# Optimization experiments

Hardware: AMD Instinct MI355X
Metric: run time of the kernel (lower is better)

## Reference

```python
import jax, jax.numpy as jnp
import numpy as np

HEAD_SIZE = 128


def setup_inputs() -> dict:
    key = jax.random.key(0)
    k0, k1, k2, k3 = jax.random.split(key, 4)
    B, S, E, H = 4, 4096, 1024, HEAD_SIZE
    x = jax.random.normal(k0, (B, S, E), dtype=jnp.float32)
    scale = 1.0 / np.sqrt(E).astype(np.float32)
    Wq = jax.random.normal(k1, (E, H), dtype=jnp.float32) * scale
    Wk = jax.random.normal(k2, (E, H), dtype=jnp.float32) * scale
    Wv = jax.random.normal(k3, (E, H), dtype=jnp.float32) * scale
    k_mask = jnp.ones((B, S), dtype=jnp.int32)
    return {"x": x, "Wq": Wq, "Wk": Wk, "Wv": Wv, "k_mask": k_mask}


def reference(x, Wq, Wk, Wv, k_mask):
    # Self-attention path (kv=None), causal=True
    Q = x @ Wq  # [B, S, H]
    K = x @ Wk  # [B, S, H]
    V = x @ Wv  # [B, S, H]
    inv_sqrt_h = np.float32(1.0 / np.sqrt(HEAD_SIZE))
    att = jnp.einsum('bqh,bkh->bqk', Q, K) * inv_sqrt_h  # [B, S, S]
    neg_inf = jnp.float32(-jnp.inf)
    # padding mask over keys: [B, 1, S_k]
    att = jnp.where(k_mask[:, None, :] == 0, neg_inf, att)
    # causal mask: tril over (q_len, k_len)
    S = Q.shape[1]
    c_mask = jnp.tril(jnp.ones((S, S), dtype=bool))  # [S, S]
    att = jnp.where(c_mask[None, :, :], att, neg_inf)
    att = jax.nn.softmax(att, axis=-1)
    return att @ V  # [B, S, H]
```

## Files before the change

### kernel.cpp

```cpp
#include <hip/hip_runtime.h>
#include <hip/hip_bf16.h>

typedef unsigned short u16;
typedef __attribute__((ext_vector_type(8))) short bf16x8;
typedef __attribute__((ext_vector_type(4))) float f32x4;
typedef __attribute__((ext_vector_type(4))) unsigned short u16x4;

#define SQ 4096
#define HQ 128
#define NCHUNK 144

__device__ __forceinline__ u16 f2b(float f) {
  unsigned int u = __float_as_uint(f);
  unsigned int r = (u + 0x7fffu + ((u >> 16) & 1u)) >> 16;
  return (u16)r;
}

__device__ __forceinline__ u16 f2b_fast(float f) {
  __hip_bfloat16 h = __float2bfloat16(f);
  return __builtin_bit_cast(u16, h);
}

__device__ __forceinline__ float b2f(u16 v) {
  unsigned int u = ((unsigned int)v) << 16;
  return __uint_as_float(u);
}

__device__ __forceinline__ void gload_lds16(const u16* gsrc, u16* ldst) {
  __builtin_amdgcn_global_load_lds((const __attribute__((address_space(1))) void*)gsrc,
                                   (__attribute__((address_space(3))) void*)ldst, 16, 0, 0);
}

__global__ __launch_bounds__(256) void k_wt(const float* __restrict__ Wq, const float* __restrict__ Wk,
                                            const float* __restrict__ Wv, u16* __restrict__ wt) {
  int idx = blockIdx.x * 256 + threadIdx.x;
  int z = idx >> 17, r = idx & 131071, n = r >> 10, k = r & 1023;
  const float* W = (z == 0) ? Wq : (z == 1) ? Wk : Wv;
  wt[idx] = f2b(W[k * 128 + n]);
}

__global__ __launch_bounds__(256, 3) void k_proj(const float* __restrict__ x, const u16* __restrict__ wt,
                                                 u16* __restrict__ qb, u16* __restrict__ kb,
                                                 u16* __restrict__ vt) {
  int blk = blockIdx.x;
  int t = threadIdx.x;
  int wn = t >> 6, lane = t & 63;
  int lr = lane & 15, lg = lane >> 4;

  __shared__ __align__(16) u16 xl[2][32 * 32];
  __shared__ __align__(16) u16 wl[2][384 * 32];

  int srow = t >> 3, sc8 = t & 7;
  const float* xg = x + (long)(blk * 32 + srow) * 1024 + sc8 * 4;
  int xch = ((sc8 >> 1) ^ ((srow >> 1) & 3));
  int xoff = srow * 32 + xch * 8 + (sc8 & 1) * 4;

  f32x4 acc[2][6];
#pragma unroll
  for (int i = 0; i < 2; ++i)
#pragma unroll
    for (int j = 0; j < 6; ++j) acc[i][j] = (f32x4){0.f, 0.f, 0.f, 0.f};

  auto stage_w = [&](int bufi, int k0) {
#pragma unroll
    for (int i = 0; i < 6; ++i) {
      int ci = i * 256 + t;
      int row = ci >> 2, ch = ci & 3;
      gload_lds16(wt + (long)row * 1024 + k0 + ((ch ^ ((row >> 1) & 3)) << 3),
                  &wl[bufi][0] + ci * 8);
    }
  };

  {
    float4 xa = *(const float4*)(xg);
    stage_w(0, 0);
    u16x4 o;
    o[0] = f2b(xa.x); o[1] = f2b(xa.y); o[2] = f2b(xa.z); o[3] = f2b(xa.w);
    *(u16x4*)(&xl[0][0] + xoff) = o;
  }
  __syncthreads();

  for (int ks = 0; ks < 32; ++ks) {
    int cur = ks & 1;
    float4 xa;
    bool more = (ks + 1 < 32);
    if (more) {
      xa = *(const float4*)(xg + (ks + 1) * 32);
      stage_w(cur ^ 1, (ks + 1) * 32);
    }
    bf16x8 af[2], bf[6];
#pragma unroll
    for (int i = 0; i < 2; ++i) {
      int row = i * 16 + lr;
      af[i] = *(const bf16x8*)(&xl[cur][0] + row * 32 + ((lg ^ ((row >> 1) & 3)) << 3));
    }
#pragma unroll
    for (int j = 0; j < 6; ++j) {
      int row = wn * 96 + j * 16 + lr;
      bf[j] = *(const bf16x8*)(&wl[cur][0] + row * 32 + ((lg ^ ((row >> 1) & 3)) << 3));
    }
#pragma unroll
    for (int i = 0; i < 2; ++i)
#pragma unroll
      for (int j = 0; j < 6; ++j)
        acc[i][j] = __builtin_amdgcn_mfma_f32_16x16x32_bf16(af[i], bf[j], acc[i][j], 0, 0, 0);
    if (more) {
      u16x4 o;
      o[0] = f2b(xa.x); o[1] = f2b(xa.y); o[2] = f2b(xa.z); o[3] = f2b(xa.w);
      *(u16x4*)(&xl[cur ^ 1][0] + xoff) = o;
    }
    __syncthreads();
  }

#pragma unroll
  for (int i = 0; i < 2; ++i)
#pragma unroll
    for (int j = 0; j < 6; ++j)
#pragma unroll
      for (int r = 0; r < 4; ++r) {
        int m = blk * 32 + i * 16 + lg * 4 + r;
        int col = wn * 96 + j * 16 + lr;
        int z = col >> 7, cz = col & 127;
        u16 v = f2b(acc[i][j][r]);
        if (z == 0) qb[(long)m * 128 + cz] = v;
        else if (z == 1) kb[(long)m * 128 + cz] = v;
        else { int bb = m >> 12, sR = m & 4095; vt[(long)bb * 524288 + (long)cz * 4096 + sR] = v; }
      }
}

__global__ __launch_bounds__(512, 4) void k_attn(const u16* __restrict__ qb, const u16* __restrict__ kb,
                                                 const u16* __restrict__ vt, const int* __restrict__ kmask,
                                                 u16* __restrict__ po, float* __restrict__ pl) {
  const float SCALE_LOG2 = 0.08838834764831845f * 1.4426950408889634f;
  const float MFIX = 24.0f;
  int f = (NCHUNK - 1) - (int)blockIdx.x;
  int b = blockIdx.y;
  int qt2 = 0, cum = 0;
  while (cum + ((qt2 + 4) >> 2) <= f) { cum += (qt2 + 4) >> 2; ++qt2; }
  int kc = f - cum;
  int ntile = 2 * qt2 + 2;
  int kt0 = kc * 8;
  int kt1 = min(kt0 + 8, ntile);

  int t = threadIdx.x, w = t >> 6, lane = t & 63;
  int lr = lane & 15, lg = lane >> 4, sw = lr & 7;
  int qrow0 = qt2 * 128 + w * 16;
  const u16* Q = qb + ((long)(b * SQ + qrow0)) * HQ;
  const u16* K = kb + (long)b * SQ * HQ;
  const u16* V = vt + (long)b * HQ * SQ;
  const int* msk = kmask + b * SQ;

  __shared__ __align__(16) u16 Kl[2][64 * 128];
  __shared__ __align__(16) u16 Vl[2][128 * 64];
  __shared__ __align__(16) u16 plds[8][16 * 64];

  bf16x8 aq[4];
#pragma unroll
  for (int c = 0; c < 4; ++c) aq[c] = *(const bf16x8*)(Q + lr * HQ + c * 32 + lg * 8);

  bf16x8 ones;
#pragma unroll
  for (int e = 0; e < 8; ++e) ones[e] = (short)0x3F80;

  f32x4 o[8];
#pragma unroll
  for (int n = 0; n < 8; ++n) o[n] = (f32x4){0.f, 0.f, 0.f, 0.f};
  f32x4 l_acc = (f32x4){0.f, 0.f, 0.f, 0.f};

  auto stage = [&](int bufi, int kb0) {
    const u16* Kg = K + (long)kb0 * HQ;
    const u16* Vg = V + kb0;
#pragma unroll
    for (int i = 0; i < 2; ++i) {
      int ci = w * 2 + i;
      int o16 = ci * 64 + lane;
      int row = o16 >> 4, ch = o16 & 15;
      gload_lds16(Kg + row * HQ + ((ch ^ (row & 7)) << 3), &Kl[bufi][ci * 512]);
    }
#pragma unroll
    for (int i = 0; i < 2; ++i) {
      int ci = w * 2 + i;
      int o16 = ci * 64 + lane;
      int row = o16 >> 3, ch = o16 & 7;
      gload_lds16(Vg + (long)row * SQ + ((ch ^ (row & 7)) << 3), &Vl[bufi][ci * 512]);
    }
  };

  stage(0, kt0 * 64);
  __syncthreads();

  u16* pw = &plds[w][0];
  for (int kt = kt0; kt < kt1; ++kt) {
    int cur = (kt - kt0) & 1;
    int kb0 = kt * 64;
    if (kt + 1 < kt1) stage(cur ^ 1, kb0 + 64);

    if (kb0 <= qrow0 + 15) {
      f32x4 s[4];
#pragma unroll
      for (int h = 0; h < 4; ++h) {
        f32x4 acc = (f32x4){0.f, 0.f, 0.f, 0.f};
        const u16* Kp = &Kl[cur][(h * 16 + lr) * 128];
#pragma unroll
        for (int c = 0; c < 4; ++c) {
          bf16x8 bk = *(const bf16x8*)(Kp + (((c * 4 + lg) ^ sw) << 3));
          acc = __builtin_amdgcn_mfma_f32_16x16x32_bf16(aq[c], bk, acc, 0, 0, 0);
        }
        s[h] = acc;
      }
      float mf[4];
#pragma unroll
      for (int h = 0; h < 4; ++h) mf[h] = (msk[kb0 + h * 16 + lr] != 0) ? 1.0f : 0.0f;
      bool needc = (kb0 + 63 > qrow0);
#pragma unroll
      for (int r = 0; r < 4; ++r) {
        int row = lg * 4 + r;
        int qr = qrow0 + row;
#pragma unroll
        for (int h = 0; h < 4; ++h) {
          float p = __builtin_exp2f(fmaf(s[h][r], SCALE_LOG2, -MFIX)) * mf[h];
          if (needc) p = ((kb0 + h * 16 + lr) <= qr) ? p : 0.0f;
          int poff = row * 64 + ((((h * 2 + (lr >> 3)) ^ (row & 7))) << 3) + (lr & 7);
          pw[poff] = f2b_fast(p);
        }
      }
      bf16x8 ap0 = *(const bf16x8*)(pw + lr * 64 + ((lg ^ sw) << 3));
      bf16x8 ap1 = *(const bf16x8*)(pw + lr * 64 + (((4 + lg) ^ sw) << 3));
      l_acc = __builtin_amdgcn_mfma_f32_16x16x32_bf16(ap0, ones, l_acc, 0, 0, 0);
      l_acc = __builtin_amdgcn_mfma_f32_16x16x32_bf16(ap1, ones, l_acc, 0, 0, 0);
#pragma unroll
      for (int n = 0; n < 8; ++n) {
        const u16* Vp = &Vl[cur][(n * 16 + lr) * 64];
        bf16x8 bv0 = *(const bf16x8*)(Vp + ((lg ^ sw) << 3));
        bf16x8 bv1 = *(const bf16x8*)(Vp + (((4 + lg) ^ sw) << 3));
        o[n] = __builtin_amdgcn_mfma_f32_16x16x32_bf16(ap0, bv0, o[n], 0, 0, 0);
        o[n] = __builtin_amdgcn_mfma_f32_16x16x32_bf16(ap1, bv1, o[n], 0, 0, 0);
      }
    }
    __syncthreads();
  }

  long p = (long)b * NCHUNK + f;
  u16* pob = po + p * 16384;
#pragma unroll
  for (int n = 0; n < 8; ++n)
#pragma unroll
    for (int r = 0; r < 4; ++r)
      pob[(w * 16 + lg * 4 + r) * 128 + n * 16 + lr] = f2b_fast(o[n][r]);
  if (lr == 0) {
#pragma unroll
    for (int r = 0; r < 4; ++r) pl[p * 128 + w * 16 + lg * 4 + r] = l_acc[r];
  }
}

__global__ __launch_bounds__(256) void k_merge(const u16* __restrict__ po, const float* __restrict__ pl,
                                               float* __restrict__ out) {
  int qt2 = blockIdx.x, b = blockIdx.y;
  int nch = (qt2 + 4) >> 2;
  int pre = 0;
  for (int q = 0; q < qt2; ++q) pre += (q + 4) >> 2;
  long pbase = (long)b * NCHUNK + pre;
  int t = threadIdx.x;
  int row = t >> 1, c0 = (t & 1) * 64;
  float l = 0.f;
  for (int i = 0; i < nch; ++i) l += pl[(pbase + i) * 128 + row];
  float inv = 1.0f / l;
  const u16* p0 = po + pbase * 16384 + row * 128 + c0;
  float* orow = out + ((long)(b * SQ + qt2 * 128 + row)) * HQ + c0;
#pragma unroll
  for (int j = 0; j < 64; j += 4) {
    float acc0 = 0.f, acc1 = 0.f, acc2 = 0.f, acc3 = 0.f;
    for (int i = 0; i < nch; ++i) {
      u16x4 v = *(const u16x4*)(p0 + (long)i * 16384 + j);
      acc0 += b2f(v[0]); acc1 += b2f(v[1]); acc2 += b2f(v[2]); acc3 += b2f(v[3]);
    }
    float4 r = {acc0 * inv, acc1 * inv, acc2 * inv, acc3 * inv};
    *(float4*)(orow + j) = r;
  }
}

extern "C" void kernel_launch(void* const* d_in, const int* in_sizes, int n_in,
                              void* d_out, int out_size, void* d_ws, size_t ws_size,
                              hipStream_t stream) {
  const float* x  = (const float*)d_in[0];
  const float* Wq = (const float*)d_in[1];
  const float* Wk = (const float*)d_in[2];
  const float* Wv = (const float*)d_in[3];
  const int* kmask = (const int*)d_in[4];
  char* ws = (char*)d_ws;
  u16* wt = (u16*)(ws + 33554432);
  u16* qb = (u16*)(ws + 34340864);
  u16* kb = (u16*)(ws + 38535168);
  u16* vt = (u16*)(ws + 42729472);
  u16* po = (u16*)ws;
  float* pl = (float*)(ws + 33554432);
  float* out = (float*)d_out;

  k_wt<<<1536, 256, 0, stream>>>(Wq, Wk, Wv, wt);
  k_proj<<<512, 256, 0, stream>>>(x, wt, qb, kb, vt);
  k_attn<<<dim3(NCHUNK, 4), 512, 0, stream>>>(qb, kb, vt, kmask, po, pl);
  k_merge<<<dim3(32, 4), 256, 0, stream>>>(po, pl, out);
}
```

Before: 136.1 us.

## Switch attention to 32x32 MFMA with register P and direct-load projection

The attention kernel now runs 4 waves, each covering 32 query rows, and uses 32x32x16 bf16 MFMA with S computed as K·Q^T. P is packed in registers with cvt_pk and permlane32 swaps, which removes the LDS round trip for P and the ones-vector MFMA used for the row sum; the row sum is now a scalar reduction. The padding mask is skipped when a wave-wide all-valid check passes. The projection kernel drops its LDS staging and reads x and W directly from global memory with 8 waves per block. The pl buffer also moves so it no longer overlaps the weight workspace. The trade-off is higher register pressure and uncoalesced direct global loads in the projection.

```diff
diff --git a/kernel.cpp b/kernel.cpp
--- a/kernel.cpp
+++ b/kernel.cpp
@@ -2,9 +2,12 @@
 #include <hip/hip_bf16.h>
 
 typedef unsigned short u16;
+typedef unsigned int u32;
 typedef __attribute__((ext_vector_type(8))) short bf16x8;
 typedef __attribute__((ext_vector_type(4))) float f32x4;
+typedef __attribute__((ext_vector_type(16))) float f32x16;
 typedef __attribute__((ext_vector_type(4))) unsigned short u16x4;
+typedef __attribute__((ext_vector_type(4))) unsigned int u32x4;
 
 #define SQ 4096
 #define HQ 128
@@ -24,6 +27,16 @@
 __device__ __forceinline__ float b2f(u16 v) {
   unsigned int u = ((unsigned int)v) << 16;
   return __uint_as_float(u);
+}
+
+__device__ __forceinline__ u32 cvtpk(float lo, float hi) {
+  u32 r;
+  asm("v_cvt_pk_bf16_f32 %0, %1, %2" : "=v"(r) : "v"(lo), "v"(hi));
+  return r;
+}
+
+__device__ __forceinline__ void pswap(u32& a, u32& b) {
+  asm("v_permlane32_swap_b32 %0, %1" : "+v"(a), "+v"(b));
 }
 
 __device__ __forceinline__ void gload_lds16(const u16* gsrc, u16* ldst) {
@@ -39,87 +52,58 @@
   wt[idx] = f2b(W[k * 128 + n]);
 }
 
-__global__ __launch_bounds__(256, 3) void k_proj(const float* __restrict__ x, const u16* __restrict__ wt,
-                                                 u16* __restrict__ qb, u16* __restrict__ kb,
-                                                 u16* __restrict__ vt) {
+__global__ __launch_bounds__(512) void k_proj(const float* __restrict__ x, const u16* __restrict__ wt,
+                                              u16* __restrict__ qb, u16* __restrict__ kb,
+                                              u16* __restrict__ vt) {
   int blk = blockIdx.x;
-  int t = threadIdx.x;
-  int wn = t >> 6, lane = t & 63;
+  int t = threadIdx.x, w = t >> 6, lane = t & 63;
   int lr = lane & 15, lg = lane >> 4;
-
-  __shared__ __align__(16) u16 xl[2][32 * 32];
-  __shared__ __align__(16) u16 wl[2][384 * 32];
-
-  int srow = t >> 3, sc8 = t & 7;
-  const float* xg = x + (long)(blk * 32 + srow) * 1024 + sc8 * 4;
-  int xch = ((sc8 >> 1) ^ ((srow >> 1) & 3));
-  int xoff = srow * 32 + xch * 8 + (sc8 & 1) * 4;
-
-  f32x4 acc[2][6];
+  int n0 = w * 48;
+
+  f32x4 acc[2][3];
 #pragma unroll
   for (int i = 0; i < 2; ++i)
 #pragma unroll
-    for (int j = 0; j < 6; ++j) acc[i][j] = (f32x4){0.f, 0.f, 0.f, 0.f};
-
-  auto stage_w = [&](int bufi, int k0) {
-#pragma unroll
-    for (int i = 0; i < 6; ++i) {
-      int ci = i * 256 + t;
-      int row = ci >> 2, ch = ci & 3;
-      gload_lds16(wt + (long)row * 1024 + k0 + ((ch ^ ((row >> 1) & 3)) << 3),
-                  &wl[bufi][0] + ci * 8);
-    }
-  };
-
-  {
-    float4 xa = *(const float4*)(xg);
-    stage_w(0, 0);
-    u16x4 o;
-    o[0] = f2b(xa.x); o[1] = f2b(xa.y); o[2] = f2b(xa.z); o[3] = f2b(xa.w);
-    *(u16x4*)(&xl[0][0] + xoff) = o;
-  }
-  __syncthreads();
-
+    for (int j = 0; j < 3; ++j) acc[i][j] = (f32x4){0.f, 0.f, 0.f, 0.f};
+
+  const float* xr = x + (long)(blk * 32 + lr) * 1024 + lg * 8;
+  const u16* wb0 = wt + (long)(n0 + lr) * 1024 + lg * 8;
+
+#pragma unroll 2
   for (int ks = 0; ks < 32; ++ks) {
-    int cur = ks & 1;
-    float4 xa;
-    bool more = (ks + 1 < 32);
-    if (more) {
-      xa = *(const float4*)(xg + (ks + 1) * 32);
-      stage_w(cur ^ 1, (ks + 1) * 32);
-    }
-    bf16x8 af[2], bf[6];
+    int k0 = ks * 32;
+    bf16x8 af[2];
 #pragma unroll
     for (int i = 0; i < 2; ++i) {
-      int row = i * 16 + lr;
-      af[i] = *(const bf16x8*)(&xl[cur][0] + row * 32 + ((lg ^ ((row >> 1) & 3)) << 3));
-    }
-#pragma unroll
-    for (int j = 0; j < 6; ++j) {
-      int row = wn * 96 + j * 16 + lr;
-      bf[j] = *(const bf16x8*)(&wl[cur][0] + row * 32 + ((lg ^ ((row >> 1) & 3)) << 3));
-    }
+      const float* ap = xr + i * 16 * 1024 + k0;
+      float4 a0 = *(const float4*)ap;
+      float4 a1 = *(const float4*)(ap + 4);
+      bf16x8 v;
+      v[0] = (short)f2b_fast(a0.x); v[1] = (short)f2b_fast(a0.y);
+      v[2] = (short)f2b_fast(a0.z); v[3] = (short)f2b_fast(a0.w);
+      v[4] = (short)f2b_fast(a1.x); v[5] = (short)f2b_fast(a1.y);
+      v[6] = (short)f2b_fast(a1.z); v[7] = (short)f2b_fast(a1.w);
+      af[i] = v;
+    }
+    bf16x8 bfr[3];
+#pragma unroll
+    for (int j = 0; j < 3; ++j)
+      bfr[j] = *(const bf16x8*)(wb0 + (long)j * 16 * 1024 + k0);
 #pragma unroll
     for (int i = 0; i < 2; ++i)
 #pragma unroll
-      for (int j = 0; j < 6; ++j)
-        acc[i][j] = __builtin_amdgcn_mfma_f32_16x16x32_bf16(af[i], bf[j], acc[i][j], 0, 0, 0);
-    if (more) {
-      u16x4 o;
-      o[0] = f2b(xa.x); o[1] = f2b(xa.y); o[2] = f2b(xa.z); o[3] = f2b(xa.w);
-      *(u16x4*)(&xl[cur ^ 1][0] + xoff) = o;
-    }
-    __syncthreads();
+      for (int j = 0; j < 3; ++j)
+        acc[i][j] = __builtin_amdgcn_mfma_f32_16x16x32_bf16(af[i], bfr[j], acc[i][j], 0, 0, 0);
   }
 
 #pragma unroll
   for (int i = 0; i < 2; ++i)
 #pragma unroll
-    for (int j = 0; j < 6; ++j)
+    for (int j = 0; j < 3; ++j)
 #pragma unroll
       for (int r = 0; r < 4; ++r) {
         int m = blk * 32 + i * 16 + lg * 4 + r;
-        int col = wn * 96 + j * 16 + lr;
+        int col = n0 + j * 16 + lr;
         int z = col >> 7, cz = col & 127;
         u16 v = f2b(acc[i][j][r]);
         if (z == 0) qb[(long)m * 128 + cz] = v;
@@ -128,9 +112,9 @@
       }
 }
 
-__global__ __launch_bounds__(512, 4) void k_attn(const u16* __restrict__ qb, const u16* __restrict__ kb,
-                                                 const u16* __restrict__ vt, const int* __restrict__ kmask,
-                                                 u16* __restrict__ po, float* __restrict__ pl) {
+__global__ __launch_bounds__(256) void k_attn(const u16* __restrict__ qb, const u16* __restrict__ kb,
+                                              const u16* __restrict__ vt, const int* __restrict__ kmask,
+                                              u16* __restrict__ po, float* __restrict__ pl) {
   const float SCALE_LOG2 = 0.08838834764831845f * 1.4426950408889634f;
   const float MFIX = 24.0f;
   int f = (NCHUNK - 1) - (int)blockIdx.x;
@@ -143,114 +127,125 @@
   int kt1 = min(kt0 + 8, ntile);
 
   int t = threadIdx.x, w = t >> 6, lane = t & 63;
-  int lr = lane & 15, lg = lane >> 4, sw = lr & 7;
-  int qrow0 = qt2 * 128 + w * 16;
-  const u16* Q = qb + ((long)(b * SQ + qrow0)) * HQ;
+  int lq = lane & 31, hh = lane >> 5;
+  int qrow0 = qt2 * 128 + w * 32;
   const u16* K = kb + (long)b * SQ * HQ;
   const u16* V = vt + (long)b * HQ * SQ;
   const int* msk = kmask + b * SQ;
 
   __shared__ __align__(16) u16 Kl[2][64 * 128];
   __shared__ __align__(16) u16 Vl[2][128 * 64];
-  __shared__ __align__(16) u16 plds[8][16 * 64];
-
-  bf16x8 aq[4];
-#pragma unroll
-  for (int c = 0; c < 4; ++c) aq[c] = *(const bf16x8*)(Q + lr * HQ + c * 32 + lg * 8);
-
-  bf16x8 ones;
-#pragma unroll
-  for (int e = 0; e < 8; ++e) ones[e] = (short)0x3F80;
-
-  f32x4 o[8];
-#pragma unroll
-  for (int n = 0; n < 8; ++n) o[n] = (f32x4){0.f, 0.f, 0.f, 0.f};
-  f32x4 l_acc = (f32x4){0.f, 0.f, 0.f, 0.f};
+
+  bf16x8 qf[8];
+  {
+    const u16* Qp = qb + (long)(b * SQ + qrow0 + lq) * HQ + hh * 8;
+#pragma unroll
+    for (int c = 0; c < 8; ++c) qf[c] = *(const bf16x8*)(Qp + c * 16);
+  }
+
+  f32x16 ot[4];
+#pragma unroll
+  for (int d = 0; d < 4; ++d) ot[d] = (f32x16)(0.f);
+  float lsum = 0.f;
 
   auto stage = [&](int bufi, int kb0) {
     const u16* Kg = K + (long)kb0 * HQ;
     const u16* Vg = V + kb0;
 #pragma unroll
-    for (int i = 0; i < 2; ++i) {
-      int ci = w * 2 + i;
-      int o16 = ci * 64 + lane;
-      int row = o16 >> 4, ch = o16 & 15;
-      gload_lds16(Kg + row * HQ + ((ch ^ (row & 7)) << 3), &Kl[bufi][ci * 512]);
-    }
-#pragma unroll
-    for (int i = 0; i < 2; ++i) {
-      int ci = w * 2 + i;
-      int o16 = ci * 64 + lane;
-      int row = o16 >> 3, ch = o16 & 7;
-      gload_lds16(Vg + (long)row * SQ + ((ch ^ (row & 7)) << 3), &Vl[bufi][ci * 512]);
+    for (int i = 0; i < 4; ++i) {
+      int cg = w * 4 + i;
+      int idx = cg * 64 + lane;
+      int row = idx >> 4, ch = idx & 15;
+      gload_lds16(Kg + row * HQ + ((ch ^ (row & 15)) << 3), &Kl[bufi][cg * 512]);
+    }
+#pragma unroll
+    for (int i = 0; i < 4; ++i) {
+      int cg = w * 4 + i;
+      int idx = cg * 64 + lane;
+      int row = idx >> 3, ch = idx & 7;
+      gload_lds16(Vg + (long)row * SQ + ((ch ^ (row & 7)) << 3), &Vl[bufi][cg * 512]);
     }
   };
 
   stage(0, kt0 * 64);
   __syncthreads();
 
-  u16* pw = &plds[w][0];
   for (int kt = kt0; kt < kt1; ++kt) {
     int cur = (kt - kt0) & 1;
     int kb0 = kt * 64;
     if (kt + 1 < kt1) stage(cur ^ 1, kb0 + 64);
 
-    if (kb0 <= qrow0 + 15) {
-      f32x4 s[4];
-#pragma unroll
-      for (int h = 0; h < 4; ++h) {
-        f32x4 acc = (f32x4){0.f, 0.f, 0.f, 0.f};
-        const u16* Kp = &Kl[cur][(h * 16 + lr) * 128];
-#pragma unroll
-        for (int c = 0; c < 4; ++c) {
-          bf16x8 bk = *(const bf16x8*)(Kp + (((c * 4 + lg) ^ sw) << 3));
-          acc = __builtin_amdgcn_mfma_f32_16x16x32_bf16(aq[c], bk, acc, 0, 0, 0);
+    if (kb0 <= qrow0 + 31) {
+      f32x16 st[2];
+#pragma unroll
+      for (int kf = 0; kf < 2; ++kf) {
+        f32x16 a = (f32x16)(0.f);
+        int krow = kf * 32 + lq;
+        const u16* Kp = &Kl[cur][krow * 128];
+        int swz = krow & 15;
+#pragma unroll
+        for (int c = 0; c < 8; ++c) {
+          bf16x8 ka = *(const bf16x8*)(Kp + (((c * 2 + hh) ^ swz) << 3));
+          a = __builtin_amdgcn_mfma_f32_32x32x16_bf16(ka, qf[c], a, 0, 0, 0);
         }
-        s[h] = acc;
+        st[kf] = a;
       }
-      float mf[4];
-#pragma unroll
-      for (int h = 0; h < 4; ++h) mf[h] = (msk[kb0 + h * 16 + lr] != 0) ? 1.0f : 0.0f;
+      int mv = msk[kb0 + lane];
+      bool allv = __all(mv != 0);
       bool needc = (kb0 + 63 > qrow0);
-#pragma unroll
-      for (int r = 0; r < 4; ++r) {
-        int row = lg * 4 + r;
-        int qr = qrow0 + row;
-#pragma unroll
-        for (int h = 0; h < 4; ++h) {
-          float p = __builtin_exp2f(fmaf(s[h][r], SCALE_LOG2, -MFIX)) * mf[h];
-          if (needc) p = ((kb0 + h * 16 + lr) <= qr) ? p : 0.0f;
-          int poff = row * 64 + ((((h * 2 + (lr >> 3)) ^ (row & 7))) << 3) + (lr & 7);
-          pw[poff] = f2b_fast(p);
+      int q = qrow0 + lq;
+      float p[32];
+#pragma unroll
+      for (int kf = 0; kf < 2; ++kf)
+#pragma unroll
+        for (int j = 0; j < 16; ++j) {
+          int keyl = kf * 32 + (j & 3) + 8 * (j >> 2) + 4 * hh;
+          int key = kb0 + keyl;
+          float pp = __builtin_exp2f(fmaf(st[kf][j], SCALE_LOG2, -MFIX));
+          if (!allv) pp = (msk[key] != 0) ? pp : 0.f;
+          if (needc) pp = (key <= q) ? pp : 0.f;
+          p[kf * 16 + j] = pp;
+          lsum += pp;
+        }
+#pragma unroll
+      for (int kk = 0; kk < 4; ++kk) {
+        int rb = (kk >> 1) * 16 + (kk & 1) * 8;
+        u32 X = cvtpk(p[rb + 0], p[rb + 1]);
+        u32 Z = cvtpk(p[rb + 2], p[rb + 3]);
+        u32 Y = cvtpk(p[rb + 4], p[rb + 5]);
+        u32 W2 = cvtpk(p[rb + 6], p[rb + 7]);
+        pswap(X, Y);
+        pswap(Z, W2);
+        u32x4 pk; pk[0] = X; pk[1] = Z; pk[2] = Y; pk[3] = W2;
+        bf16x8 pb = __builtin_bit_cast(bf16x8, pk);
+#pragma unroll
+        for (int d = 0; d < 4; ++d) {
+          int vrow = d * 32 + lq;
+          bf16x8 va = *(const bf16x8*)(&Vl[cur][vrow * 64 + (((kk * 2 + hh) ^ (vrow & 7)) << 3)]);
+          ot[d] = __builtin_amdgcn_mfma_f32_32x32x16_bf16(va, pb, ot[d], 0, 0, 0);
         }
       }
-      bf16x8 ap0 = *(const bf16x8*)(pw + lr * 64 + ((lg ^ sw) << 3));
-      bf16x8 ap1 = *(const bf16x8*)(pw + lr * 64 + (((4 + lg) ^ sw) << 3));
-      l_acc = __builtin_amdgcn_mfma_f32_16x16x32_bf16(ap0, ones, l_acc, 0, 0, 0);
-      l_acc = __builtin_amdgcn_mfma_f32_16x16x32_bf16(ap1, ones, l_acc, 0, 0, 0);
-#pragma unroll
-      for (int n = 0; n < 8; ++n) {
-        const u16* Vp = &Vl[cur][(n * 16 + lr) * 64];
-        bf16x8 bv0 = *(const bf16x8*)(Vp + ((lg ^ sw) << 3));
-        bf16x8 bv1 = *(const bf16x8*)(Vp + (((4 + lg) ^ sw) << 3));
-        o[n] = __builtin_amdgcn_mfma_f32_16x16x32_bf16(ap0, bv0, o[n], 0, 0, 0);
-        o[n] = __builtin_amdgcn_mfma_f32_16x16x32_bf16(ap1, bv1, o[n], 0, 0, 0);
-      }
     }
     __syncthreads();
   }
 
-  long p = (long)b * NCHUNK + f;
-  u16* pob = po + p * 16384;
-#pragma unroll
-  for (int n = 0; n < 8; ++n)
-#pragma unroll
-    for (int r = 0; r < 4; ++r)
-      pob[(w * 16 + lg * 4 + r) * 128 + n * 16 + lr] = f2b_fast(o[n][r]);
-  if (lr == 0) {
-#pragma unroll
-    for (int r = 0; r < 4; ++r) pl[p * 128 + w * 16 + lg * 4 + r] = l_acc[r];
-  }
+  lsum += __shfl_xor(lsum, 32);
+  long pbi = (long)b * NCHUNK + f;
+  u16* pob = po + pbi * 16384;
+  int qloc = w * 32 + lq;
+#pragma unroll
+  for (int d = 0; d < 4; ++d)
+#pragma unroll
+    for (int g = 0; g < 4; ++g) {
+      int d0 = d * 32 + 8 * g + 4 * hh;
+      u16x4 vv;
+      vv[0] = f2b_fast(ot[d][4 * g + 0]);
+      vv[1] = f2b_fast(ot[d][4 * g + 1]);
+      vv[2] = f2b_fast(ot[d][4 * g + 2]);
+      vv[3] = f2b_fast(ot[d][4 * g + 3]);
+      *(u16x4*)(pob + (long)qloc * 128 + d0) = vv;
+    }
+  if (hh == 0) pl[pbi * 128 + qloc] = lsum;
 }
 
 __global__ __launch_bounds__(256) void k_merge(const u16* __restrict__ po, const float* __restrict__ pl,
@@ -293,11 +288,11 @@
   u16* kb = (u16*)(ws + 38535168);
   u16* vt = (u16*)(ws + 42729472);
   u16* po = (u16*)ws;
-  float* pl = (float*)(ws + 33554432);
+  float* pl = (float*)(ws + 33554432 - 2359296);
   float* out = (float*)d_out;
 
   k_wt<<<1536, 256, 0, stream>>>(Wq, Wk, Wv, wt);
-  k_proj<<<512, 256, 0, stream>>>(x, wt, qb, kb, vt);
-  k_attn<<<dim3(NCHUNK, 4), 512, 0, stream>>>(qb, kb, vt, kmask, po, pl);
+  k_proj<<<512, 512, 0, stream>>>(x, wt, qb, kb, vt);
+  k_attn<<<dim3(NCHUNK, 4), 256, 0, stream>>>(qb, kb, vt, kmask, po, pl);
   k_merge<<<dim3(32, 4), 256, 0, stream>>>(po, pl, out);
 }
```

Result: slower. 231.7 us (+70.2%).
